# Optimization experiments

Hardware: AMD Instinct MI355X
Metric: run time of the kernel (lower is better)

## Reference

```python
import jax, jax.numpy as jnp
import numpy as np
from jax import lax

TEMPERATURES = (0.05, 0.1, 0.2)
MASK_SELF = True


def _cdist(a, b):
    # Euclidean distance matrix [Na, Nb], matches torch.cdist(p=2)
    d2 = (jnp.sum(a * a, axis=1)[:, None]
          + jnp.sum(b * b, axis=1)[None, :]
          - 2.0 * (a @ b.T))
    return jnp.sqrt(jnp.maximum(d2, 0.0))


def setup_inputs() -> dict:
    key = jax.random.key(0)
    k1, k2, k3 = jax.random.split(key, 3)
    N, N_pos, D = 4096, 4096, 256
    x = jax.random.normal(k1, (N, D), dtype=jnp.float32)
    y_pos = jax.random.normal(k2, (N_pos, D), dtype=jnp.float32)
    y_neg = jax.random.normal(k3, (N, D), dtype=jnp.float32)
    return {"x": x, "y_pos": y_pos, "y_neg": y_neg}


def reference(x, y_pos, y_neg):
    N, D = x.shape
    N_neg = y_neg.shape[0]

    dist_pos = _cdist(x, y_pos)            # [N, N_pos]
    dist_neg = _cdist(x, y_neg)            # [N, N_neg]
    if MASK_SELF:
        dist_neg = dist_neg + jnp.eye(N, dtype=x.dtype) * 1e6

    # temperature auto-scale, detached in original (torch.no_grad)
    mean_dist = lax.stop_gradient(jnp.mean(dist_pos))

    dist = jnp.concatenate([dist_neg, dist_pos], axis=1)  # [N, N_neg+N_pos]

    V_total = jnp.zeros_like(x)
    for T in TEMPERATURES:
        adaptive_T = T * mean_dist
        log_kernel = jnp.maximum(-dist / adaptive_T, -80.0)
        kernel = jnp.exp(log_kernel)
        row_sum = jnp.sum(kernel, axis=-1, keepdims=True)   # [N, 1]
        col_sum = jnp.sum(kernel, axis=-2, keepdims=True)   # [1, N_neg+N_pos]
        normalizer = jnp.sqrt(jnp.maximum(row_sum * col_sum, 1e-12))
        A = kernel / normalizer
        A_neg = A[:, :N_neg]
        A_pos = A[:, N_neg:]
        # second-order reweighting
        W_pos = A_pos * jnp.sum(A_neg, axis=-1, keepdims=True)
        W_neg = A_neg * jnp.sum(A_pos, axis=-1, keepdims=True)
        V_total = V_total + (W_pos @ y_pos - W_neg @ y_neg)

    target = lax.stop_gradient(x + V_total)
    loss = jnp.mean((x - target) ** 2)
    return loss
```

## Files before the change

kernel.cpp:

```cpp
#include <hip/hip_runtime.h>

#define NROWS 4096
#define DCOLS 8192
#define DIM   256
#define NHALF 4096

typedef __attribute__((ext_vector_type(8))) short bf16x8;
typedef __attribute__((ext_vector_type(4))) float f32x4;
typedef __attribute__((ext_vector_type(4))) unsigned short ushort4v;
typedef __attribute__((ext_vector_type(8))) unsigned short ushort8v;
typedef __attribute__((ext_vector_type(8))) _Float16 half8;

static __device__ __forceinline__ unsigned short f2bf(float f) {
  union { float f; unsigned int i; } v; v.f = f;
  unsigned int x = v.i;
  return (unsigned short)((x + 0x7fffu + ((x >> 16) & 1u)) >> 16);
}

static __device__ __forceinline__ void gload_lds16(const void* g, void* l) {
  __builtin_amdgcn_global_load_lds(
      (const __attribute__((address_space(1))) void*)g,
      (__attribute__((address_space(3))) void*)l, 16, 0, 0);
}

#define WREDUCE(v) { v += __shfl_xor(v, 1); v += __shfl_xor(v, 2); v += __shfl_xor(v, 4); \
                     v += __shfl_xor(v, 8); v += __shfl_xor(v, 16); v += __shfl_xor(v, 32); }

__global__ __launch_bounds__(256) void k_prep(
    const float* __restrict__ x, const float* __restrict__ ypos,
    const float* __restrict__ yneg, unsigned short* __restrict__ xb,
    unsigned short* __restrict__ yb, float* __restrict__ xx, float* __restrict__ yy) {
  const int lane = threadIdx.x & 63, w = threadIdx.x >> 6;
  const int b = blockIdx.x * 4 + w;
  const float* src; unsigned short* dst; float* nrm;
  if (b < 4096)      { src = x + (size_t)b * DIM;             dst = xb + (size_t)b * DIM;            nrm = xx + b; }
  else if (b < 8192) { int r = b - 4096; src = yneg + (size_t)r * DIM; dst = yb + (size_t)r * DIM;   nrm = yy + r; }
  else               { int r = b - 8192; src = ypos + (size_t)r * DIM; dst = yb + (size_t)(NHALF + r) * DIM; nrm = yy + NHALF + r; }
  float4 v = *(const float4*)(src + lane * 4);
  ushort4v ov = { f2bf(v.x), f2bf(v.y), f2bf(v.z), f2bf(v.w) };
  *(ushort4v*)(dst + lane * 4) = ov;
  float s = v.x * v.x + v.y * v.y + v.z * v.z + v.w * v.w;
  WREDUCE(s);
  if (lane == 0) nrm[0] = s;
}

__global__ __launch_bounds__(256) void k_transpose(
    const unsigned short* __restrict__ yb, unsigned short* __restrict__ ybt) {
  __shared__ unsigned short tile[64][68];
  int r0 = blockIdx.x * 64;
  int c0 = blockIdx.y * 64;
  int tx = threadIdx.x & 63, ty = threadIdx.x >> 6;
  #pragma unroll
  for (int it = 0; it < 16; ++it) {
    int r = it * 4 + ty;
    tile[r][tx] = yb[(size_t)(r0 + r) * DIM + c0 + tx];
  }
  __syncthreads();
  #pragma unroll
  for (int it = 0; it < 16; ++it) {
    int c = it * 4 + ty;
    ybt[(size_t)(c0 + c) * DCOLS + r0 + tx] = tile[tx][c];
  }
}

__global__ __launch_bounds__(256) void k_mean(
    const unsigned short* __restrict__ xb, const unsigned short* __restrict__ yb,
    const float* __restrict__ xx, const float* __restrict__ yy,
    double* __restrict__ meanacc) {
  __shared__ unsigned short As[128 * 64];
  __shared__ unsigned short Bs[128 * 64];
  __shared__ float red[4];
  const int bj = NHALF + blockIdx.x * 128;
  const int bi = blockIdx.y * 128;
  const int tid = threadIdx.x;
  const int lane = tid & 63, wid = tid >> 6;
  const int wr = wid >> 1, wc = wid & 1;
  f32x4 acc[4][4];
  #pragma unroll
  for (int m = 0; m < 4; ++m)
    #pragma unroll
    for (int n = 0; n < 4; ++n) acc[m][n] = (f32x4){0.f, 0.f, 0.f, 0.f};

  for (int k0 = 0; k0 < DIM; k0 += 64) {
    __syncthreads();
    #pragma unroll
    for (int it = 0; it < 4; ++it) {
      int L = it * 256 + tid;
      int row = L >> 3;
      int cb = (L & 7) * 16;
      int cbs = cb ^ ((row & 7) << 4);
      gload_lds16(xb + (size_t)(bi + row) * DIM + k0 + (cbs >> 1), (char*)As + L * 16);
      gload_lds16(yb + (size_t)(bj + row) * DIM + k0 + (cbs >> 1), (char*)Bs + L * 16);
    }
    __syncthreads();
    #pragma unroll
    for (int kk = 0; kk < 2; ++kk) {
      bf16x8 a[4], b[4];
      #pragma unroll
      for (int m = 0; m < 4; ++m) {
        int row = wr * 64 + m * 16 + (lane & 15);
        int cb = (kk * 64 + ((lane >> 4) * 16)) ^ ((row & 7) << 4);
        a[m] = *(const bf16x8*)((const char*)As + row * 128 + cb);
      }
      #pragma unroll
      for (int n = 0; n < 4; ++n) {
        int row = wc * 64 + n * 16 + (lane & 15);
        int cb = (kk * 64 + ((lane >> 4) * 16)) ^ ((row & 7) << 4);
        b[n] = *(const bf16x8*)((const char*)Bs + row * 128 + cb);
      }
      #pragma unroll
      for (int m = 0; m < 4; ++m)
        #pragma unroll
        for (int n = 0; n < 4; ++n)
          acc[m][n] = __builtin_amdgcn_mfma_f32_16x16x32_bf16(a[m], b[n], acc[m][n], 0, 0, 0);
    }
  }

  float xv[16], yv[4];
  #pragma unroll
  for (int m = 0; m < 4; ++m)
    #pragma unroll
    for (int r = 0; r < 4; ++r)
      xv[m * 4 + r] = xx[bi + wr * 64 + m * 16 + (lane >> 4) * 4 + r];
  #pragma unroll
  for (int n = 0; n < 4; ++n)
    yv[n] = yy[bj + wc * 64 + n * 16 + (lane & 15)];

  float lsum = 0.f;
  #pragma unroll
  for (int m = 0; m < 4; ++m)
    #pragma unroll
    for (int n = 0; n < 4; ++n)
      #pragma unroll
      for (int r = 0; r < 4; ++r) {
        float d2 = xv[m * 4 + r] + yv[n] - 2.f * acc[m][n][r];
        lsum += sqrtf(fmaxf(d2, 0.f));
      }
  WREDUCE(lsum);
  if (lane == 0) red[wid] = lsum;
  __syncthreads();
  if (tid == 0) atomicAdd(meanacc, (double)(red[0] + red[1] + red[2] + red[3]));
}

__global__ __launch_bounds__(256) void k_diste(
    const unsigned short* __restrict__ xb, const unsigned short* __restrict__ yb,
    const float* __restrict__ xx, const float* __restrict__ yy,
    const double* __restrict__ meanacc, unsigned short* __restrict__ ebuf,
    float* __restrict__ cs_part) {
  __shared__ __align__(16) char lds[32768];
  unsigned short* As = (unsigned short*)lds;
  unsigned short* Bs = (unsigned short*)(lds + 16384);
  const int bj = blockIdx.x * 128;
  const int bi = blockIdx.y * 128;
  const int tid = threadIdx.x;
  const int lane = tid & 63, wid = tid >> 6;
  const int wr = wid >> 1, wc = wid & 1;
  f32x4 acc[4][4];
  #pragma unroll
  for (int m = 0; m < 4; ++m)
    #pragma unroll
    for (int n = 0; n < 4; ++n) acc[m][n] = (f32x4){0.f, 0.f, 0.f, 0.f};

  for (int k0 = 0; k0 < DIM; k0 += 64) {
    __syncthreads();
    #pragma unroll
    for (int it = 0; it < 4; ++it) {
      int L = it * 256 + tid;
      int row = L >> 3;
      int cb = (L & 7) * 16;
      int cbs = cb ^ ((row & 7) << 4);
      gload_lds16(xb + (size_t)(bi + row) * DIM + k0 + (cbs >> 1), (char*)As + L * 16);
      gload_lds16(yb + (size_t)(bj + row) * DIM + k0 + (cbs >> 1), (char*)Bs + L * 16);
    }
    __syncthreads();
    #pragma unroll
    for (int kk = 0; kk < 2; ++kk) {
      bf16x8 a[4], b[4];
      #pragma unroll
      for (int m = 0; m < 4; ++m) {
        int row = wr * 64 + m * 16 + (lane & 15);
        int cb = (kk * 64 + ((lane >> 4) * 16)) ^ ((row & 7) << 4);
        a[m] = *(const bf16x8*)((const char*)As + row * 128 + cb);
      }
      #pragma unroll
      for (int n = 0; n < 4; ++n) {
        int row = wc * 64 + n * 16 + (lane & 15);
        int cb = (kk * 64 + ((lane >> 4) * 16)) ^ ((row & 7) << 4);
        b[n] = *(const bf16x8*)((const char*)Bs + row * 128 + cb);
      }
      #pragma unroll
      for (int m = 0; m < 4; ++m)
        #pragma unroll
        for (int n = 0; n < 4; ++n)
          acc[m][n] = __builtin_amdgcn_mfma_f32_16x16x32_bf16(a[m], b[n], acc[m][n], 0, 0, 0);
    }
  }

  const float md = (float)(meanacc[0] * (1.0 / 16777216.0));
  const float ia2 = 1.f / (0.2f * md);
  float xv[16], yv[4];
  #pragma unroll
  for (int m = 0; m < 4; ++m)
    #pragma unroll
    for (int r = 0; r < 4; ++r)
      xv[m * 4 + r] = xx[bi + wr * 64 + m * 16 + (lane >> 4) * 4 + r];
  #pragma unroll
  for (int n = 0; n < 4; ++n)
    yv[n] = yy[bj + wc * 64 + n * 16 + (lane & 15)];

  __syncthreads();

  float cq[3][4];
  #pragma unroll
  for (int p = 0; p < 3; ++p)
    #pragma unroll
    for (int n = 0; n < 4; ++n) cq[p][n] = 0.f;

  #pragma unroll
  for (int m = 0; m < 4; ++m) {
    #pragma unroll
    for (int n = 0; n < 4; ++n) {
      int col = wc * 64 + n * 16 + (lane & 15);
      int gj = bj + col;
      #pragma unroll
      for (int r = 0; r < 4; ++r) {
        int row = wr * 64 + m * 16 + (lane >> 4) * 4 + r;
        int gi = bi + row;
        float d2 = xv[m * 4 + r] + yv[n] - 2.f * acc[m][n][r];
        float d = sqrtf(fmaxf(d2, 0.f));
        float q = __expf(-d * ia2);
        if (gi == gj) q = 0.f;
        float q2 = q * q;
        cq[2][n] += q; cq[1][n] += q2; cq[0][n] += q2 * q2;
        *(_Float16*)(lds + row * 256 + ((col * 2) ^ ((row & 7) << 4))) = (_Float16)q;
      }
    }
  }
  #pragma unroll
  for (int p = 0; p < 3; ++p)
    #pragma unroll
    for (int n = 0; n < 4; ++n) {
      float v = cq[p][n];
      v += __shfl_xor(v, 16); v += __shfl_xor(v, 32);
      cq[p][n] = v;
    }
  if (lane < 16) {
    const int slab = blockIdx.y * 2 + wr;
    #pragma unroll
    for (int p = 0; p < 3; ++p)
      #pragma unroll
      for (int n = 0; n < 4; ++n)
        cs_part[(size_t)slab * 24576 + p * 8192 + bj + wc * 64 + n * 16 + lane] = cq[p][n];
  }
  __syncthreads();
  _Float16* dp = (_Float16*)ebuf;
  #pragma unroll 4
  for (int it = 0; it < 32; ++it) {
    int row = it * 4 + wid;
    unsigned int v = *(const unsigned int*)(lds + row * 256 + ((lane * 4) ^ ((row & 7) << 4)));
    *(unsigned int*)(dp + (size_t)(bi + row) * DCOLS + bj + lane * 2) = v;
  }
}

__global__ __launch_bounds__(256) void k_csred(
    const float* __restrict__ cs_part, _Float16* __restrict__ ich) {
  int idx = blockIdx.x * 256 + threadIdx.x;
  float s = 0.f;
  #pragma unroll 8
  for (int sl = 0; sl < 64; ++sl) s += cs_part[(size_t)sl * 24576 + idx];
  ich[idx] = (_Float16)rsqrtf(s);
}

__global__ __launch_bounds__(256) void k_rowstat(
    const unsigned short* __restrict__ ebuf, const _Float16* __restrict__ ich,
    float* __restrict__ gtab) {
  __shared__ float red[4][9];
  const int i = blockIdx.x;
  const int t = threadIdx.x;
  const int lane = t & 63, w = t >> 6;
  const _Float16* erow = (const _Float16*)(ebuf + (size_t)i * DCOLS);
  float r0 = 0, r1 = 0, r2 = 0, sn0 = 0, sn1 = 0, sn2 = 0, sp0 = 0, sp1 = 0, sp2 = 0;
  #pragma unroll
  for (int it = 0; it < 4; ++it) {
    int j0 = it * 2048 + t * 8;
    half8 e8 = *(const half8*)(erow + j0);
    half8 c0v = *(const half8*)(ich + j0);
    half8 c1v = *(const half8*)(ich + 8192 + j0);
    half8 c2v = *(const half8*)(ich + 16384 + j0);
    float a0 = 0, a1 = 0, a2 = 0, b0 = 0, b1 = 0, b2 = 0;
    #pragma unroll
    for (int u = 0; u < 8; ++u) {
      float q = (float)e8[u];
      float q2 = q * q, q4 = q2 * q2;
      b0 += q4; b1 += q2; b2 += q;
      a0 += q4 * (float)c0v[u];
      a1 += q2 * (float)c1v[u];
      a2 += q  * (float)c2v[u];
    }
    r0 += b0; r1 += b1; r2 += b2;
    if (it < 2) { sn0 += a0; sn1 += a1; sn2 += a2; }
    else        { sp0 += a0; sp1 += a1; sp2 += a2; }
  }
  WREDUCE(r0); WREDUCE(r1); WREDUCE(r2);
  WREDUCE(sn0); WREDUCE(sn1); WREDUCE(sn2);
  WREDUCE(sp0); WREDUCE(sp1); WREDUCE(sp2);
  if (lane == 0) {
    red[w][0] = r0; red[w][1] = r1; red[w][2] = r2;
    red[w][3] = sn0; red[w][4] = sn1; red[w][5] = sn2;
    red[w][6] = sp0; red[w][7] = sp1; red[w][8] = sp2;
  }
  __syncthreads();
  if (t < 9) {
    float v = red[0][t] + red[1][t] + red[2][t] + red[3][t];
    red[0][t] = v;
  }
  __syncthreads();
  if (t < 3) {
    float R = red[0][t], Sn = red[0][3 + t], Sp = red[0][6 + t];
    gtab[i * 8 + t] = -Sp / R;
    gtab[i * 8 + 4 + t] = Sn / R;
  }
}

__global__ __launch_bounds__(512) void k_flash(
    const unsigned short* __restrict__ ebuf, const unsigned short* __restrict__ ybt,
    const _Float16* __restrict__ ich, const float* __restrict__ gtab,
    _Float16* __restrict__ vpart) {
  __shared__ __align__(16) char lds[40960];
  unsigned short* Ct = (unsigned short*)lds;
  unsigned short* Bs = (unsigned short*)(lds + 8192);
  const int jc = blockIdx.x;
  const int rb = blockIdx.y;
  const int j0base = jc * 1024;
  const int tid = threadIdx.x;
  const int lane = tid & 63, wid = tid >> 6;
  const int wr = wid >> 2, wc = wid & 3;
  const int crow = tid >> 3;
  const int cj8 = (tid & 7) * 8;
  const float* gp = gtab + (size_t)(rb * 64 + crow) * 8 + (jc < 4 ? 0 : 4);
  const float g0 = gp[0], g1 = gp[1], g2 = gp[2];
  const _Float16* erowp = (const _Float16*)ebuf + (size_t)(rb * 64 + crow) * DCOLS;

  f32x4 acc[2][4];
  #pragma unroll
  for (int m = 0; m < 2; ++m)
    #pragma unroll
    for (int n = 0; n < 4; ++n) acc[m][n] = (f32x4){0.f, 0.f, 0.f, 0.f};

  for (int jt = 0; jt < 16; ++jt) {
    const int j0 = j0base + jt * 64;
    __syncthreads();
    #pragma unroll
    for (int it = 0; it < 4; ++it) {
      int L = it * 512 + tid;
      int row = L >> 3;
      int cb = (L & 7) * 16;
      int cbs = cb ^ ((row & 7) << 4);
      gload_lds16(ybt + (size_t)row * DCOLS + j0 + (cbs >> 1), (char*)Bs + L * 16);
    }
    {
      half8 e8 = *(const half8*)(erowp + j0 + cj8);
      half8 c0v = *(const half8*)(ich + j0 + cj8);
      half8 c1v = *(const half8*)(ich + 8192 + j0 + cj8);
      half8 c2v = *(const half8*)(ich + 16384 + j0 + cj8);
      ushort8v outv;
      #pragma unroll
      for (int u = 0; u < 8; ++u) {
        float q = (float)e8[u];
        float q2 = q * q, q4 = q2 * q2;
        float C = q4 * (float)c0v[u] * g0 + q2 * (float)c1v[u] * g1 + q * (float)c2v[u] * g2;
        outv[u] = f2bf(C);
      }
      *(ushort8v*)((char*)Ct + crow * 128 + ((cj8 * 2) ^ ((crow & 7) << 4))) = outv;
    }
    __syncthreads();
    #pragma unroll
    for (int kk = 0; kk < 2; ++kk) {
      bf16x8 a[2], b[4];
      #pragma unroll
      for (int m = 0; m < 2; ++m) {
        int row = wr * 32 + m * 16 + (lane & 15);
        int cb = (kk * 64 + ((lane >> 4) * 16)) ^ ((row & 7) << 4);
        a[m] = *(const bf16x8*)((const char*)Ct + row * 128 + cb);
      }
      #pragma unroll
      for (int n = 0; n < 4; ++n) {
        int row = wc * 64 + n * 16 + (lane & 15);
        int cb = (kk * 64 + ((lane >> 4) * 16)) ^ ((row & 7) << 4);
        b[n] = *(const bf16x8*)((const char*)Bs + row * 128 + cb);
      }
      #pragma unroll
      for (int m = 0; m < 2; ++m)
        #pragma unroll
        for (int n = 0; n < 4; ++n)
          acc[m][n] = __builtin_amdgcn_mfma_f32_16x16x32_bf16(a[m], b[n], acc[m][n], 0, 0, 0);
    }
  }
  #pragma unroll
  for (int m = 0; m < 2; ++m)
    #pragma unroll
    for (int n = 0; n < 4; ++n)
      #pragma unroll
      for (int r = 0; r < 4; ++r) {
        int gi = rb * 64 + wr * 32 + m * 16 + (lane >> 4) * 4 + r;
        int gd = wc * 64 + n * 16 + (lane & 15);
        vpart[(size_t)jc * 1048576 + (size_t)gi * 256 + gd] = (_Float16)acc[m][n][r];
      }
}

__global__ __launch_bounds__(256) void k_loss(
    const _Float16* __restrict__ vpart, float* __restrict__ ploss) {
  const int tid = blockIdx.x * 256 + threadIdx.x;
  const size_t e0 = (size_t)tid * 8;
  float vv[8] = {0, 0, 0, 0, 0, 0, 0, 0};
  #pragma unroll
  for (int sl = 0; sl < 8; ++sl) {
    half8 h = *(const half8*)(vpart + (size_t)sl * 1048576 + e0);
    #pragma unroll
    for (int u = 0; u < 8; ++u) vv[u] += (float)h[u];
  }
  float s = 0.f;
  #pragma unroll
  for (int u = 0; u < 8; ++u) s += vv[u] * vv[u];
  WREDUCE(s);
  __shared__ float red[4];
  if ((threadIdx.x & 63) == 0) red[threadIdx.x >> 6] = s;
  __syncthreads();
  if (threadIdx.x == 0) ploss[blockIdx.x] = red[0] + red[1] + red[2] + red[3];
}

__global__ __launch_bounds__(256) void k_finish(
    const float* __restrict__ ploss, float* __restrict__ out) {
  float v = ploss[threadIdx.x] + ploss[threadIdx.x + 256];
  WREDUCE(v);
  __shared__ float red[4];
  if ((threadIdx.x & 63) == 0) red[threadIdx.x >> 6] = v;
  __syncthreads();
  if (threadIdx.x == 0)
    out[0] = (float)((double)(red[0] + red[1] + red[2] + red[3]) / 1048576.0);
}

extern "C" void kernel_launch(void* const* d_in, const int* in_sizes, int n_in,
                              void* d_out, int out_size, void* d_ws, size_t ws_size,
                              hipStream_t stream) {
  (void)in_sizes; (void)n_in; (void)out_size; (void)ws_size;
  const float* x    = (const float*)d_in[0];
  const float* ypos = (const float*)d_in[1];
  const float* yneg = (const float*)d_in[2];

  char* ws = (char*)d_ws;
  size_t o = 0;
  unsigned short* dist = (unsigned short*)(ws + o); o += (size_t)NROWS * DCOLS * 2;
  unsigned short* xb   = (unsigned short*)(ws + o); o += (size_t)NROWS * DIM * 2;
  unsigned short* yb   = (unsigned short*)(ws + o); o += (size_t)DCOLS * DIM * 2;
  unsigned short* ybt  = (unsigned short*)(ws + o); o += (size_t)DCOLS * DIM * 2;
  float* xx      = (float*)(ws + o); o += NROWS * 4;
  float* yy      = (float*)(ws + o); o += DCOLS * 4;
  double* meanacc = (double*)(ws + o); o += 256;
  _Float16* ich  = (_Float16*)(ws + o); o += 3 * DCOLS * 2;
  float* gtab    = (float*)(ws + o); o += (size_t)NROWS * 8 * 4;
  float* ploss   = (float*)(ws + o); o += 512 * 4;
  float* cs_part = (float*)(ws + o);
  _Float16* vpart = (_Float16*)(ws + o); o += (size_t)8 * NROWS * DIM * 2;

  hipMemsetAsync(meanacc, 0, 8, stream);
  k_prep<<<3072, 256, 0, stream>>>(x, ypos, yneg, xb, yb, xx, yy);
  k_transpose<<<dim3(128, 4), 256, 0, stream>>>(yb, ybt);
  k_mean<<<dim3(32, 32), 256, 0, stream>>>(xb, yb, xx, yy, meanacc);
  k_diste<<<dim3(64, 32), 256, 0, stream>>>(xb, yb, xx, yy, meanacc, dist, cs_part);
  k_csred<<<96, 256, 0, stream>>>(cs_part, ich);
  k_rowstat<<<4096, 256, 0, stream>>>(dist, ich, gtab);
  k_flash<<<dim3(8, 64), 512, 0, stream>>>(dist, ybt, ich, gtab, vpart);
  k_loss<<<512, 256, 0, stream>>>(vpart, ploss);
  k_finish<<<1, 256, 0, stream>>>(ploss, (float*)d_out);
}
```

Baseline: 154.5 us.

## Move kernel-weight math to packed fp16 with pre-scaled exponentials and fp16 MFMA

```diff
diff --git a/kernel.cpp b/kernel.cpp
--- a/kernel.cpp
+++ b/kernel.cpp
@@ -9,7 +9,11 @@
 typedef __attribute__((ext_vector_type(4))) float f32x4;
 typedef __attribute__((ext_vector_type(4))) unsigned short ushort4v;
 typedef __attribute__((ext_vector_type(8))) unsigned short ushort8v;
+typedef __attribute__((ext_vector_type(2))) _Float16 half2v;
+typedef __attribute__((ext_vector_type(4))) _Float16 half4v;
 typedef __attribute__((ext_vector_type(8))) _Float16 half8;
+
+#define LN128 4.852030263919617f
 
 static __device__ __forceinline__ unsigned short f2bf(float f) {
   union { float f; unsigned int i; } v; v.f = f;
@@ -17,35 +21,51 @@
   return (unsigned short)((x + 0x7fffu + ((x >> 16) & 1u)) >> 16);
 }
 
+static __device__ __forceinline__ half2v cvt_pk(float a, float b) {
+  return __builtin_bit_cast(half2v, __builtin_amdgcn_cvt_pkrtz(a, b));
+}
+
 static __device__ __forceinline__ void gload_lds16(const void* g, void* l) {
   __builtin_amdgcn_global_load_lds(
       (const __attribute__((address_space(1))) void*)g,
       (__attribute__((address_space(3))) void*)l, 16, 0, 0);
 }
 
+static __device__ __forceinline__ float hsum8(half8 v) {
+  float s = 0.f;
+  #pragma unroll
+  for (int u = 0; u < 8; ++u) s += (float)v[u];
+  return s;
+}
+
 #define WREDUCE(v) { v += __shfl_xor(v, 1); v += __shfl_xor(v, 2); v += __shfl_xor(v, 4); \
                      v += __shfl_xor(v, 8); v += __shfl_xor(v, 16); v += __shfl_xor(v, 32); }
 
 __global__ __launch_bounds__(256) void k_prep(
     const float* __restrict__ x, const float* __restrict__ ypos,
     const float* __restrict__ yneg, unsigned short* __restrict__ xb,
-    unsigned short* __restrict__ yb, float* __restrict__ xx, float* __restrict__ yy) {
+    unsigned short* __restrict__ yb, _Float16* __restrict__ yh,
+    float* __restrict__ xx, float* __restrict__ yy) {
   const int lane = threadIdx.x & 63, w = threadIdx.x >> 6;
   const int b = blockIdx.x * 4 + w;
-  const float* src; unsigned short* dst; float* nrm;
+  const float* src; unsigned short* dst; float* nrm; size_t yoff = 0; bool isy = false;
   if (b < 4096)      { src = x + (size_t)b * DIM;             dst = xb + (size_t)b * DIM;            nrm = xx + b; }
-  else if (b < 8192) { int r = b - 4096; src = yneg + (size_t)r * DIM; dst = yb + (size_t)r * DIM;   nrm = yy + r; }
-  else               { int r = b - 8192; src = ypos + (size_t)r * DIM; dst = yb + (size_t)(NHALF + r) * DIM; nrm = yy + NHALF + r; }
+  else if (b < 8192) { int r = b - 4096; src = yneg + (size_t)r * DIM; dst = yb + (size_t)r * DIM;   nrm = yy + r; yoff = (size_t)r * DIM; isy = true; }
+  else               { int r = b - 8192; src = ypos + (size_t)r * DIM; dst = yb + (size_t)(NHALF + r) * DIM; nrm = yy + NHALF + r; yoff = (size_t)(NHALF + r) * DIM; isy = true; }
   float4 v = *(const float4*)(src + lane * 4);
   ushort4v ov = { f2bf(v.x), f2bf(v.y), f2bf(v.z), f2bf(v.w) };
   *(ushort4v*)(dst + lane * 4) = ov;
+  if (isy) {
+    half4v hv = { (_Float16)v.x, (_Float16)v.y, (_Float16)v.z, (_Float16)v.w };
+    *(half4v*)(yh + yoff + lane * 4) = hv;
+  }
   float s = v.x * v.x + v.y * v.y + v.z * v.z + v.w * v.w;
   WREDUCE(s);
   if (lane == 0) nrm[0] = s;
 }
 
 __global__ __launch_bounds__(256) void k_transpose(
-    const unsigned short* __restrict__ yb, unsigned short* __restrict__ ybt) {
+    const unsigned short* __restrict__ yhsrc, unsigned short* __restrict__ ybt) {
   __shared__ unsigned short tile[64][68];
   int r0 = blockIdx.x * 64;
   int c0 = blockIdx.y * 64;
@@ -53,7 +73,7 @@
   #pragma unroll
   for (int it = 0; it < 16; ++it) {
     int r = it * 4 + ty;
-    tile[r][tx] = yb[(size_t)(r0 + r) * DIM + c0 + tx];
+    tile[r][tx] = yhsrc[(size_t)(r0 + r) * DIM + c0 + tx];
   }
   __syncthreads();
   #pragma unroll
@@ -166,8 +186,8 @@
     #pragma unroll
     for (int it = 0; it < 4; ++it) {
       int L = it * 256 + tid;
+      int cb = (L & 7) * 16;
       int row = L >> 3;
-      int cb = (L & 7) * 16;
       int cbs = cb ^ ((row & 7) << 4);
       gload_lds16(xb + (size_t)(bi + row) * DIM + k0 + (cbs >> 1), (char*)As + L * 16);
       gload_lds16(yb + (size_t)(bj + row) * DIM + k0 + (cbs >> 1), (char*)Bs + L * 16);
@@ -208,41 +228,55 @@
   for (int n = 0; n < 4; ++n)
     yv[n] = yy[bj + wc * 64 + n * 16 + (lane & 15)];
 
-  __syncthreads();
-
-  float cq[3][4];
-  #pragma unroll
-  for (int p = 0; p < 3; ++p)
-    #pragma unroll
-    for (int n = 0; n < 4; ++n) cq[p][n] = 0.f;
-
+  const bool hasdiag = (bi == bj);
+  __syncthreads();
+
+  half2v cq4[4] = {}, cq2[4] = {}, cq1[4] = {};
   #pragma unroll
   for (int m = 0; m < 4; ++m) {
+    const int r0 = wr * 64 + m * 16 + (lane >> 4) * 4;
     #pragma unroll
     for (int n = 0; n < 4; ++n) {
-      int col = wc * 64 + n * 16 + (lane & 15);
-      int gj = bj + col;
+      const int col = wc * 64 + n * 16 + (lane & 15);
+      float q[4];
       #pragma unroll
       for (int r = 0; r < 4; ++r) {
-        int row = wr * 64 + m * 16 + (lane >> 4) * 4 + r;
-        int gi = bi + row;
         float d2 = xv[m * 4 + r] + yv[n] - 2.f * acc[m][n][r];
         float d = sqrtf(fmaxf(d2, 0.f));
-        float q = __expf(-d * ia2);
-        if (gi == gj) q = 0.f;
-        float q2 = q * q;
-        cq[2][n] += q; cq[1][n] += q2; cq[0][n] += q2 * q2;
-        *(_Float16*)(lds + row * 256 + ((col * 2) ^ ((row & 7) << 4))) = (_Float16)q;
-      }
-    }
+        q[r] = __expf(fmaf(d, -ia2, LN128));
+      }
+      if (hasdiag) {
+        #pragma unroll
+        for (int r = 0; r < 4; ++r)
+          if (r0 + r == col) q[r] = 0.f;
+      }
+      half2v p01 = cvt_pk(q[0], q[1]);
+      half2v p23 = cvt_pk(q[2], q[3]);
+      half2v q2a = p01 * p01, q2b = p23 * p23;
+      half2v q4a = q2a * q2a, q4b = q2b * q2b;
+      cq1[n] += p01; cq1[n] += p23;
+      cq2[n] += q2a; cq2[n] += q2b;
+      cq4[n] += q4a; cq4[n] += q4b;
+      *(_Float16*)(lds + (r0 + 0) * 256 + ((col * 2) ^ (((r0 + 0) & 7) << 4))) = p01[0];
+      *(_Float16*)(lds + (r0 + 1) * 256 + ((col * 2) ^ (((r0 + 1) & 7) << 4))) = p01[1];
+      *(_Float16*)(lds + (r0 + 2) * 256 + ((col * 2) ^ (((r0 + 2) & 7) << 4))) = p23[0];
+      *(_Float16*)(lds + (r0 + 3) * 256 + ((col * 2) ^ (((r0 + 3) & 7) << 4))) = p23[1];
+    }
+  }
+  float csf[3][4];
+  #pragma unroll
+  for (int n = 0; n < 4; ++n) {
+    csf[0][n] = (float)cq4[n][0] + (float)cq4[n][1];
+    csf[1][n] = (float)cq2[n][0] + (float)cq2[n][1];
+    csf[2][n] = (float)cq1[n][0] + (float)cq1[n][1];
   }
   #pragma unroll
   for (int p = 0; p < 3; ++p)
     #pragma unroll
     for (int n = 0; n < 4; ++n) {
-      float v = cq[p][n];
+      float v = csf[p][n];
       v += __shfl_xor(v, 16); v += __shfl_xor(v, 32);
-      cq[p][n] = v;
+      csf[p][n] = v;
     }
   if (lane < 16) {
     const int slab = blockIdx.y * 2 + wr;
@@ -250,7 +284,7 @@
     for (int p = 0; p < 3; ++p)
       #pragma unroll
       for (int n = 0; n < 4; ++n)
-        cs_part[(size_t)slab * 24576 + p * 8192 + bj + wc * 64 + n * 16 + lane] = cq[p][n];
+        cs_part[(size_t)slab * 24576 + p * 8192 + bj + wc * 64 + n * 16 + lane] = csf[p][n];
   }
   __syncthreads();
   _Float16* dp = (_Float16*)ebuf;
@@ -279,41 +313,33 @@
   const int t = threadIdx.x;
   const int lane = t & 63, w = t >> 6;
   const _Float16* erow = (const _Float16*)(ebuf + (size_t)i * DCOLS);
-  float r0 = 0, r1 = 0, r2 = 0, sn0 = 0, sn1 = 0, sn2 = 0, sp0 = 0, sp1 = 0, sp2 = 0;
+  half8 r4a = {}, r2a = {}, r1a = {};
+  half8 sn4 = {}, sn2 = {}, sn1 = {}, sp4 = {}, sp2 = {}, sp1 = {};
   #pragma unroll
   for (int it = 0; it < 4; ++it) {
     int j0 = it * 2048 + t * 8;
-    half8 e8 = *(const half8*)(erow + j0);
-    half8 c0v = *(const half8*)(ich + j0);
-    half8 c1v = *(const half8*)(ich + 8192 + j0);
-    half8 c2v = *(const half8*)(ich + 16384 + j0);
-    float a0 = 0, a1 = 0, a2 = 0, b0 = 0, b1 = 0, b2 = 0;
-    #pragma unroll
-    for (int u = 0; u < 8; ++u) {
-      float q = (float)e8[u];
-      float q2 = q * q, q4 = q2 * q2;
-      b0 += q4; b1 += q2; b2 += q;
-      a0 += q4 * (float)c0v[u];
-      a1 += q2 * (float)c1v[u];
-      a2 += q  * (float)c2v[u];
-    }
-    r0 += b0; r1 += b1; r2 += b2;
-    if (it < 2) { sn0 += a0; sn1 += a1; sn2 += a2; }
-    else        { sp0 += a0; sp1 += a1; sp2 += a2; }
-  }
-  WREDUCE(r0); WREDUCE(r1); WREDUCE(r2);
-  WREDUCE(sn0); WREDUCE(sn1); WREDUCE(sn2);
-  WREDUCE(sp0); WREDUCE(sp1); WREDUCE(sp2);
+    half8 e = *(const half8*)(erow + j0);
+    half8 e2 = e * e, e4 = e2 * e2;
+    half8 c0 = *(const half8*)(ich + j0);
+    half8 c1 = *(const half8*)(ich + 8192 + j0);
+    half8 c2 = *(const half8*)(ich + 16384 + j0);
+    r4a += e4; r2a += e2; r1a += e;
+    if (it < 2) { sn4 += e4 * c0; sn2 += e2 * c1; sn1 += e * c2; }
+    else        { sp4 += e4 * c0; sp2 += e2 * c1; sp1 += e * c2; }
+  }
+  float v0 = hsum8(r4a), v1 = hsum8(r2a), v2 = hsum8(r1a);
+  float v3 = hsum8(sn4), v4 = hsum8(sn2), v5 = hsum8(sn1);
+  float v6 = hsum8(sp4), v7 = hsum8(sp2), v8 = hsum8(sp1);
+  WREDUCE(v0); WREDUCE(v1); WREDUCE(v2);
+  WREDUCE(v3); WREDUCE(v4); WREDUCE(v5);
+  WREDUCE(v6); WREDUCE(v7); WREDUCE(v8);
   if (lane == 0) {
-    red[w][0] = r0; red[w][1] = r1; red[w][2] = r2;
-    red[w][3] = sn0; red[w][4] = sn1; red[w][5] = sn2;
-    red[w][6] = sp0; red[w][7] = sp1; red[w][8] = sp2;
-  }
-  __syncthreads();
-  if (t < 9) {
-    float v = red[0][t] + red[1][t] + red[2][t] + red[3][t];
-    red[0][t] = v;
-  }
+    red[w][0] = v0; red[w][1] = v1; red[w][2] = v2;
+    red[w][3] = v3; red[w][4] = v4; red[w][5] = v5;
+    red[w][6] = v6; red[w][7] = v7; red[w][8] = v8;
+  }
+  __syncthreads();
+  if (t < 9) red[0][t] = red[0][t] + red[1][t] + red[2][t] + red[3][t];
   __syncthreads();
   if (t < 3) {
     float R = red[0][t], Sn = red[0][3 + t], Sp = red[0][6 + t];
@@ -327,8 +353,6 @@
     const _Float16* __restrict__ ich, const float* __restrict__ gtab,
     _Float16* __restrict__ vpart) {
   __shared__ __align__(16) char lds[40960];
-  unsigned short* Ct = (unsigned short*)lds;
-  unsigned short* Bs = (unsigned short*)(lds + 8192);
   const int jc = blockIdx.x;
   const int rb = blockIdx.y;
   const int j0base = jc * 1024;
@@ -338,7 +362,10 @@
   const int crow = tid >> 3;
   const int cj8 = (tid & 7) * 8;
   const float* gp = gtab + (size_t)(rb * 64 + crow) * 8 + (jc < 4 ? 0 : 4);
-  const float g0 = gp[0], g1 = gp[1], g2 = gp[2];
+  const _Float16 g0h = (_Float16)gp[0], g1h = (_Float16)gp[1], g2h = (_Float16)gp[2];
+  const half8 g0v = {g0h, g0h, g0h, g0h, g0h, g0h, g0h, g0h};
+  const half8 g1v = {g1h, g1h, g1h, g1h, g1h, g1h, g1h, g1h};
+  const half8 g2v = {g2h, g2h, g2h, g2h, g2h, g2h, g2h, g2h};
   const _Float16* erowp = (const _Float16*)ebuf + (size_t)(rb * 64 + crow) * DCOLS;
 
   f32x4 acc[2][4];
@@ -356,44 +383,38 @@
       int row = L >> 3;
       int cb = (L & 7) * 16;
       int cbs = cb ^ ((row & 7) << 4);
-      gload_lds16(ybt + (size_t)row * DCOLS + j0 + (cbs >> 1), (char*)Bs + L * 16);
+      gload_lds16(ybt + (size_t)row * DCOLS + j0 + (cbs >> 1), lds + 8192 + L * 16);
     }
     {
-      half8 e8 = *(const half8*)(erowp + j0 + cj8);
-      half8 c0v = *(const half8*)(ich + j0 + cj8);
-      half8 c1v = *(const half8*)(ich + 8192 + j0 + cj8);
-      half8 c2v = *(const half8*)(ich + 16384 + j0 + cj8);
-      ushort8v outv;
-      #pragma unroll
-      for (int u = 0; u < 8; ++u) {
-        float q = (float)e8[u];
-        float q2 = q * q, q4 = q2 * q2;
-        float C = q4 * (float)c0v[u] * g0 + q2 * (float)c1v[u] * g1 + q * (float)c2v[u] * g2;
-        outv[u] = f2bf(C);
-      }
-      *(ushort8v*)((char*)Ct + crow * 128 + ((cj8 * 2) ^ ((crow & 7) << 4))) = outv;
+      half8 e = *(const half8*)(erowp + j0 + cj8);
+      half8 e2 = e * e, e4 = e2 * e2;
+      half8 c0 = *(const half8*)(ich + j0 + cj8);
+      half8 c1 = *(const half8*)(ich + 8192 + j0 + cj8);
+      half8 c2 = *(const half8*)(ich + 16384 + j0 + cj8);
+      half8 C8 = (e4 * c0) * g0v + (e2 * c1) * g1v + (e * c2) * g2v;
+      *(half8*)(lds + crow * 128 + ((cj8 * 2) ^ ((crow & 7) << 4))) = C8;
     }
     __syncthreads();
     #pragma unroll
     for (int kk = 0; kk < 2; ++kk) {
-      bf16x8 a[2], b[4];
+      half8 a[2], b[4];
       #pragma unroll
       for (int m = 0; m < 2; ++m) {
         int row = wr * 32 + m * 16 + (lane & 15);
         int cb = (kk * 64 + ((lane >> 4) * 16)) ^ ((row & 7) << 4);
-        a[m] = *(const bf16x8*)((const char*)Ct + row * 128 + cb);
+        a[m] = *(const half8*)(lds + row * 128 + cb);
       }
       #pragma unroll
       for (int n = 0; n < 4; ++n) {
         int row = wc * 64 + n * 16 + (lane & 15);
         int cb = (kk * 64 + ((lane >> 4) * 16)) ^ ((row & 7) << 4);
-        b[n] = *(const bf16x8*)((const char*)Bs + row * 128 + cb);
+        b[n] = *(const half8*)(lds + 8192 + row * 128 + cb);
       }
       #pragma unroll
       for (int m = 0; m < 2; ++m)
         #pragma unroll
         for (int n = 0; n < 4; ++n)
-          acc[m][n] = __builtin_amdgcn_mfma_f32_16x16x32_bf16(a[m], b[n], acc[m][n], 0, 0, 0);
+          acc[m][n] = __builtin_amdgcn_mfma_f32_16x16x32_f16(a[m], b[n], acc[m][n], 0, 0, 0);
     }
   }
   #pragma unroll
@@ -460,12 +481,13 @@
   _Float16* ich  = (_Float16*)(ws + o); o += 3 * DCOLS * 2;
   float* gtab    = (float*)(ws + o); o += (size_t)NROWS * 8 * 4;
   float* ploss   = (float*)(ws + o); o += 512 * 4;
+  _Float16* yh   = (_Float16*)(ws + o);
   float* cs_part = (float*)(ws + o);
   _Float16* vpart = (_Float16*)(ws + o); o += (size_t)8 * NROWS * DIM * 2;
 
   hipMemsetAsync(meanacc, 0, 8, stream);
-  k_prep<<<3072, 256, 0, stream>>>(x, ypos, yneg, xb, yb, xx, yy);
-  k_transpose<<<dim3(128, 4), 256, 0, stream>>>(yb, ybt);
+  k_prep<<<3072, 256, 0, stream>>>(x, ypos, yneg, xb, yb, yh, xx, yy);
+  k_transpose<<<dim3(128, 4), 256, 0, stream>>>((const unsigned short*)yh, ybt);
   k_mean<<<dim3(32, 32), 256, 0, stream>>>(xb, yb, xx, yy, meanacc);
   k_diste<<<dim3(64, 32), 256, 0, stream>>>(xb, yb, xx, yy, meanacc, dist, cs_part);
   k_csred<<<96, 256, 0, stream>>>(cs_part, ich);
```

Measured after the change: 151.6 us. About the same (-1.9%).
